# Performance work log

Measured on AMD Instinct MI355X. Metric: run time of the kernel, lower is better.

## Reference

```python
import jax, jax.numpy as jnp
import numpy as np

D_MODEL, N_HEADS, D_K, D_V, D_FF, SEQ = 2048, 16, 128, 128, 8192, 2048
EPS = 1e-5


def _layernorm(x, g, b):
    mu = jnp.mean(x, axis=-1, keepdims=True)
    var = jnp.var(x, axis=-1, keepdims=True)
    return (x - mu) * jax.lax.rsqrt(var + EPS) * g + b


def setup_inputs() -> dict:
    key = jax.random.key(0)
    ks = jax.random.split(key, 10)
    return {
        "x": jax.random.normal(ks[0], (SEQ, D_MODEL), jnp.float32),
        # per-head projections stacked over heads (matches num_heads separate DotProductAttention params)
        "wq": jax.random.normal(ks[1], (N_HEADS, D_MODEL, D_K), jnp.float32),
        "wk": jax.random.normal(ks[2], (N_HEADS, D_MODEL, D_K), jnp.float32),
        "wv": jax.random.normal(ks[3], (N_HEADS, D_MODEL, D_V), jnp.float32),
        "w_proj": jax.random.normal(ks[4], (N_HEADS * D_V, D_MODEL), jnp.float32),
        "g1": jnp.ones((D_MODEL,), jnp.float32),
        "b1": jnp.zeros((D_MODEL,), jnp.float32),
        "fc1_w": jax.random.normal(ks[5], (D_MODEL, D_FF), jnp.float32) * 0.02,
        "fc1_b": jnp.zeros((D_FF,), jnp.float32),
        "fc2_w": jax.random.normal(ks[6], (D_FF, D_MODEL), jnp.float32) * 0.02,
        "fc2_b": jnp.zeros((D_MODEL,), jnp.float32),
        "g2": jnp.ones((D_MODEL,), jnp.float32),
        "b2": jnp.zeros((D_MODEL,), jnp.float32),
    }


def reference(x, wq, wk, wv, w_proj, g1, b1, fc1_w, fc1_b, fc2_w, fc2_b, g2, b2):
    # multi-head attention (heads batched via einsum; same math as the per-head loop)
    q = jnp.einsum("sd,hdk->hsk", x, wq)
    k = jnp.einsum("sd,hdk->hsk", x, wk)
    v = jnp.einsum("sd,hdv->hsv", x, wv)
    scores = jnp.einsum("hsk,htk->hst", q, k) * (1.0 / np.sqrt(D_K))
    attn = jax.nn.softmax(scores, axis=-1)
    heads = jnp.einsum("hst,htv->hsv", attn, v)  # [H,S,Dv]
    concat = jnp.transpose(heads, (1, 0, 2)).reshape(SEQ, N_HEADS * D_V)
    attn_out = concat @ w_proj
    # residual + LayerNorm (dropout=0 -> identity)
    h = _layernorm(x + attn_out, g1, b1)
    # FFN with ReLU
    ff = jax.nn.relu(h @ fc1_w + fc1_b) @ fc2_w + fc2_b
    return _layernorm(h + ff, g2, b2)
```

## Files before the change

kernel.cpp:

```cpp
#include <hip/hip_runtime.h>


typedef __bf16 bf16;
typedef __attribute__((ext_vector_type(8))) __bf16 bf16x8;
typedef __attribute__((ext_vector_type(4))) __bf16 bf16x4;
typedef __attribute__((ext_vector_type(4))) float f32x4;
typedef __attribute__((ext_vector_type(4))) unsigned int u32x4;

#define MFMA(a, b, c) __builtin_amdgcn_mfma_f32_16x16x32_bf16((a), (b), (c), 0, 0, 0)
#define NEG_INF (-3.402823466e38f)

__device__ __forceinline__ void cp16(void* lds, const void* g) {
  __builtin_amdgcn_global_load_lds(
      (const __attribute__((address_space(1))) unsigned int*)g,
      (__attribute__((address_space(3))) unsigned int*)lds, 16, 0, 0);
}

#define SBAR() __builtin_amdgcn_sched_barrier(0)
#define GBAR()                              \
  do {                                      \
    asm volatile("" ::: "memory");          \
    __builtin_amdgcn_s_barrier();           \
    asm volatile("" ::: "memory");          \
  } while (0)
#define LGKM0()                                         \
  do {                                                  \
    asm volatile("s_waitcnt lgkmcnt(0)" ::: "memory");  \
    __builtin_amdgcn_sched_barrier(0);                  \
  } while (0)
#define VMC6()                                          \
  do {                                                  \
    asm volatile("s_waitcnt vmcnt(6)" ::: "memory");    \
    __builtin_amdgcn_sched_barrier(0);                  \
  } while (0)


__global__ void k_split_x(const float* __restrict__ x, bf16* __restrict__ xh,
                          bf16* __restrict__ xl) {
  int i = blockIdx.x * 256 + threadIdx.x;
  f32x4 v = ((const f32x4*)x)[i];
  bf16x4 h, l;
#pragma unroll
  for (int j = 0; j < 4; ++j) {
    bf16 hi = (bf16)v[j];
    h[j] = hi;
    l[j] = (bf16)(v[j] - (float)hi);
  }
  ((bf16x4*)xh)[i] = h;
  ((bf16x4*)xl)[i] = l;
}

template <bool SPLIT>
__global__ void k_tcvt(const float* __restrict__ in, bf16* __restrict__ oh,
                       bf16* __restrict__ ol, int R, int C) {
  __shared__ float t[64][65];
  long zoff = (long)blockIdx.z * R * C;
  int c0 = blockIdx.x * 64, r0 = blockIdx.y * 64;
  int cc = threadIdx.x & 63, rr = threadIdx.x >> 6;
#pragma unroll
  for (int i = 0; i < 16; ++i) {
    int r = i * 4 + rr;
    t[r][cc] = in[zoff + (long)(r0 + r) * C + c0 + cc];
  }
  __syncthreads();
#pragma unroll
  for (int i = 0; i < 16; ++i) {
    int orow = i * 4 + rr;
    float v = t[cc][orow];
    long oidx = zoff + (long)(c0 + orow) * R + r0 + cc;
    bf16 hi = (bf16)v;
    oh[oidx] = hi;
    if (SPLIT) ol[oidx] = (bf16)(v - (float)hi);
  }
}

__global__ void k_combine4(const float* __restrict__ p, long pstr,
                           bf16* __restrict__ o) {
  int i = blockIdx.x * 256 + threadIdx.x;
  f32x4 v = ((const f32x4*)p)[i];
#pragma unroll
  for (int zz = 1; zz < 4; ++zz) v += ((const f32x4*)(p + zz * pstr))[i];
  bf16x4 ob;
#pragma unroll
  for (int j = 0; j < 4; ++j) ob[j] = (bf16)v[j];
  ((bf16x4*)o)[i] = ob;
}

template <int EPI>
__global__ __launch_bounds__(512, 1) void k_gemm8(
    const bf16* __restrict__ A, const bf16* __restrict__ B,
    float* __restrict__ Cf, bf16* __restrict__ Cb,
    const float* __restrict__ bias, int M, int N, int K, int nsplit) {
  __shared__ char lds[131072];
  const int tid = threadIdx.x, w = tid >> 6, l = tid & 63;
  const int l16 = l & 15, lg = l >> 4;
  const int wr = w >> 2, wc = w & 3;
  const long bm0 = (long)blockIdx.y * 256, bn0 = (long)blockIdx.x * 256;
  const int z = blockIdx.z;
  const int ksz = K / nsplit, kbeg = z * ksz;
  const int nt = ksz >> 6;
  const long lK = K;

  const int srow = w * 8 + (l >> 3);
  const int sslot = (l & 7) ^ (l >> 3);

  auto STAGE = [&](int bufp, int isB, int h, int tt) {
    int tc = tt < nt ? tt : nt - 1;
    char* dst = lds + bufp * 65536 + isB * 32768 + h * 16384 + w * 1024;
    const bf16* G = isB ? B : A;
    long r0 = (isB ? bn0 : bm0) + h * 128 + srow;
    const bf16* src = G + r0 * lK + kbeg + tc * 64 + sslot * 8;
    cp16(dst, src);
    cp16(dst + 8192, src + 64 * lK);
  };
  auto LDA = [&](int bufp, int mf, int ks) -> bf16x8 {
    int inrow = (mf & 3) * 32 + wr * 16 + l16;
    int byo = bufp * 65536 + (mf >> 2) * 16384 + inrow * 128 +
              ((((ks << 2) + lg) ^ (inrow & 7)) << 4);
    return *(const bf16x8*)(lds + byo);
  };
  auto LDB = [&](int bufp, int nf, int ks) -> bf16x8 {
    int inrow = (nf & 1) * 64 + wc * 16 + l16;
    int byo = bufp * 65536 + 32768 + (nf >> 1) * 16384 + inrow * 128 +
              ((((ks << 2) + lg) ^ (inrow & 7)) << 4);
    return *(const bf16x8*)(lds + byo);
  };

  f32x4 acc[8][4];
#pragma unroll
  for (int mf = 0; mf < 8; ++mf)
#pragma unroll
    for (int nf = 0; nf < 4; ++nf)
#pragma unroll
      for (int j = 0; j < 4; ++j) acc[mf][nf][j] = 0.f;

  STAGE(0, 0, 0, 0);
  STAGE(0, 1, 0, 0);
  STAGE(0, 0, 1, 0);
  STAGE(0, 1, 1, 0);
  STAGE(1, 1, 0, 1);
  STAGE(1, 0, 1, 1);
  STAGE(1, 1, 1, 1);
  SBAR();
  VMC6();
  GBAR();

  bf16x8 a[4][2], b[2][2];
  for (int t = 0; t < nt; ++t) {
    const int cb = t & 1, nb = cb ^ 1;
#pragma unroll
    for (int mf = 0; mf < 4; ++mf)
#pragma unroll
      for (int ks = 0; ks < 2; ++ks) a[mf][ks] = LDA(cb, mf, ks);
#pragma unroll
    for (int nf = 0; nf < 2; ++nf)
#pragma unroll
      for (int ks = 0; ks < 2; ++ks) b[nf][ks] = LDB(cb, nf, ks);
    STAGE(nb, 0, 0, t + 1);
    SBAR();
    GBAR();
    LGKM0();
    __builtin_amdgcn_s_setprio(1);
#pragma unroll
    for (int mf = 0; mf < 4; ++mf)
#pragma unroll
      for (int nf = 0; nf < 2; ++nf)
#pragma unroll
        for (int ks = 0; ks < 2; ++ks)
          acc[mf][nf] = MFMA(a[mf][ks], b[nf][ks], acc[mf][nf]);
    __builtin_amdgcn_s_setprio(0);
    GBAR();
#pragma unroll
    for (int mf = 0; mf < 4; ++mf)
#pragma unroll
      for (int ks = 0; ks < 2; ++ks) a[mf][ks] = LDA(cb, mf + 4, ks);
    STAGE(cb, 1, 0, t + 2);
    SBAR();
    GBAR();
    LGKM0();
    __builtin_amdgcn_s_setprio(1);
#pragma unroll
    for (int mf = 0; mf < 4; ++mf)
#pragma unroll
      for (int nf = 0; nf < 2; ++nf)
#pragma unroll
        for (int ks = 0; ks < 2; ++ks)
          acc[mf + 4][nf] = MFMA(a[mf][ks], b[nf][ks], acc[mf + 4][nf]);
    __builtin_amdgcn_s_setprio(0);
    GBAR();
#pragma unroll
    for (int nf = 0; nf < 2; ++nf)
#pragma unroll
      for (int ks = 0; ks < 2; ++ks) b[nf][ks] = LDB(cb, nf + 2, ks);
    GBAR();
    LGKM0();
    __builtin_amdgcn_s_setprio(1);
#pragma unroll
    for (int mf = 0; mf < 4; ++mf)
#pragma unroll
      for (int nf = 0; nf < 2; ++nf)
#pragma unroll
        for (int ks = 0; ks < 2; ++ks)
          acc[mf + 4][nf + 2] = MFMA(a[mf][ks], b[nf][ks], acc[mf + 4][nf + 2]);
    __builtin_amdgcn_s_setprio(0);
    GBAR();
#pragma unroll
    for (int mf = 0; mf < 4; ++mf)
#pragma unroll
      for (int ks = 0; ks < 2; ++ks) a[mf][ks] = LDA(cb, mf, ks);
    STAGE(cb, 0, 1, t + 2);
    STAGE(cb, 1, 1, t + 2);
    SBAR();
    VMC6();
    GBAR();
    LGKM0();
    __builtin_amdgcn_s_setprio(1);
#pragma unroll
    for (int mf = 0; mf < 4; ++mf)
#pragma unroll
      for (int nf = 0; nf < 2; ++nf)
#pragma unroll
        for (int ks = 0; ks < 2; ++ks)
          acc[mf][nf + 2] = MFMA(a[mf][ks], b[nf][ks], acc[mf][nf + 2]);
    __builtin_amdgcn_s_setprio(0);
    GBAR();
  }
  asm volatile("s_waitcnt vmcnt(0) lgkmcnt(0)" ::: "memory");

#pragma unroll
  for (int mf = 0; mf < 8; ++mf)
#pragma unroll
    for (int nf = 0; nf < 4; ++nf) {
      long col = bn0 + nf * 64 + wc * 16 + l16;
      float bv = (EPI == 2) ? bias[col] : 0.f;
#pragma unroll
      for (int jj = 0; jj < 4; ++jj) {
        long row = bm0 + mf * 32 + wr * 16 + lg * 4 + jj;
        float v = acc[mf][nf][jj];
        if (EPI == 0) {
          Cf[(long)z * M * N + row * N + col] = v;
        } else {
          v = fmaxf(v + bv, 0.f);
          Cb[row * N + col] = (bf16)v;
        }
      }
    }
}

__global__ __launch_bounds__(512, 1) void k_split8(
    const bf16* __restrict__ Ah_g, const bf16* __restrict__ Al_g,
    const bf16* __restrict__ Bh_g, const bf16* __restrict__ Bl_g,
    bf16* __restrict__ Ch, bf16* __restrict__ Cl,
    int M, int N, int K, float scale, int scale_ncols) {
  __shared__ char lds[98304];
  const int tid = threadIdx.x, w = tid >> 6, l = tid & 63;
  const int l16 = l & 15, lg = l >> 4;
  const int wr = w >> 2, wc = w & 3;
  const long bm0 = (long)blockIdx.y * 128, bn0 = (long)blockIdx.x * 256;
  const int nt = K >> 5;
  const long lK = K;

  const int srcrow = tid >> 2;
  const int ss = (tid & 3) ^ ((tid >> 3) & 3);

  auto STG_A = [&](int bufp, int isLo, int tt) {
    int tc = tt < nt ? tt : nt - 1;
    char* dst = lds + bufp * 49152 + isLo * 8192 + tid * 16;
    const bf16* G = isLo ? Al_g : Ah_g;
    cp16(dst, &G[(bm0 + srcrow) * lK + tc * 32 + ss * 8]);
  };
  auto STG_B = [&](int bufp, int isLo, int half, int tt) {
    int tc = tt < nt ? tt : nt - 1;
    char* dst = lds + bufp * 49152 + 16384 + isLo * 16384 + half * 8192 + tid * 16;
    const bf16* G = isLo ? Bl_g : Bh_g;
    cp16(dst, &G[(bn0 + half * 128 + srcrow) * lK + tc * 32 + ss * 8]);
  };
  auto LDA8 = [&](int bufp, int mf, int isLo) -> bf16x8 {
    int row = mf * 32 + wr * 16 + l16;
    int byo = bufp * 49152 + isLo * 8192 + row * 64 +
              ((lg ^ ((row >> 1) & 3)) << 4);
    return *(const bf16x8*)(lds + byo);
  };
  auto LDB8 = [&](int bufp, int nf, int isLo) -> bf16x8 {
    int row = nf * 64 + wc * 16 + l16;
    int byo = bufp * 49152 + 16384 + isLo * 16384 + row * 64 +
              ((lg ^ ((row >> 1) & 3)) << 4);
    return *(const bf16x8*)(lds + byo);
  };

  f32x4 acc[4][4];
#pragma unroll
  for (int mf = 0; mf < 4; ++mf)
#pragma unroll
    for (int nf = 0; nf < 4; ++nf)
#pragma unroll
      for (int j = 0; j < 4; ++j) acc[mf][nf][j] = 0.f;

  STG_B(0, 0, 0, 0); STG_B(0, 1, 0, 0);
  STG_A(0, 0, 0);    STG_A(0, 1, 0);
  STG_B(0, 0, 1, 0); STG_B(0, 1, 1, 0);
  STG_B(1, 0, 0, 1); STG_B(1, 1, 0, 1);
  STG_A(1, 0, 1);    STG_A(1, 1, 1);
  STG_B(1, 0, 1, 1); STG_B(1, 1, 1, 1);
  SBAR();
  VMC6();
  GBAR();

  bf16x8 ah[4], al[4], bh[2], bl[2];
  for (int t = 0; t < nt; ++t) {
    const int cb = t & 1;
#pragma unroll
    for (int mf = 0; mf < 2; ++mf) {
      ah[mf] = LDA8(cb, mf, 0);
      al[mf] = LDA8(cb, mf, 1);
    }
#pragma unroll
    for (int nf = 0; nf < 2; ++nf) {
      bh[nf] = LDB8(cb, nf, 0);
      bl[nf] = LDB8(cb, nf, 1);
    }
    SBAR();
    GBAR();
    LGKM0();
    __builtin_amdgcn_s_setprio(1);
#pragma unroll
    for (int mf = 0; mf < 2; ++mf)
#pragma unroll
      for (int nf = 0; nf < 2; ++nf) {
        acc[mf][nf] = MFMA(ah[mf], bh[nf], acc[mf][nf]);
        acc[mf][nf] = MFMA(ah[mf], bl[nf], acc[mf][nf]);
        acc[mf][nf] = MFMA(al[mf], bh[nf], acc[mf][nf]);
      }
    __builtin_amdgcn_s_setprio(0);
    GBAR();
#pragma unroll
    for (int mf = 2; mf < 4; ++mf) {
      ah[mf] = LDA8(cb, mf, 0);
      al[mf] = LDA8(cb, mf, 1);
    }
    STG_B(cb, 0, 0, t + 2);
    STG_B(cb, 1, 0, t + 2);
    SBAR();
    GBAR();
    LGKM0();
    __builtin_amdgcn_s_setprio(1);
#pragma unroll
    for (int mf = 2; mf < 4; ++mf)
#pragma unroll
      for (int nf = 0; nf < 2; ++nf) {
        acc[mf][nf] = MFMA(ah[mf], bh[nf], acc[mf][nf]);
        acc[mf][nf] = MFMA(ah[mf], bl[nf], acc[mf][nf]);
        acc[mf][nf] = MFMA(al[mf], bh[nf], acc[mf][nf]);
      }
    __builtin_amdgcn_s_setprio(0);
    GBAR();
#pragma unroll
    for (int nf = 0; nf < 2; ++nf) {
      bh[nf] = LDB8(cb, nf + 2, 0);
      bl[nf] = LDB8(cb, nf + 2, 1);
    }
    STG_A(cb, 0, t + 2);
    STG_A(cb, 1, t + 2);
    SBAR();
    GBAR();
    LGKM0();
    __builtin_amdgcn_s_setprio(1);
#pragma unroll
    for (int mf = 2; mf < 4; ++mf)
#pragma unroll
      for (int nf = 0; nf < 2; ++nf) {
        acc[mf][nf + 2] = MFMA(ah[mf], bh[nf], acc[mf][nf + 2]);
        acc[mf][nf + 2] = MFMA(ah[mf], bl[nf], acc[mf][nf + 2]);
        acc[mf][nf + 2] = MFMA(al[mf], bh[nf], acc[mf][nf + 2]);
      }
    __builtin_amdgcn_s_setprio(0);
    GBAR();
    STG_B(cb, 0, 1, t + 2);
    STG_B(cb, 1, 1, t + 2);
    SBAR();
    VMC6();
    GBAR();
    __builtin_amdgcn_s_setprio(1);
#pragma unroll
    for (int mf = 0; mf < 2; ++mf)
#pragma unroll
      for (int nf = 0; nf < 2; ++nf) {
        acc[mf][nf + 2] = MFMA(ah[mf], bh[nf], acc[mf][nf + 2]);
        acc[mf][nf + 2] = MFMA(ah[mf], bl[nf], acc[mf][nf + 2]);
        acc[mf][nf + 2] = MFMA(al[mf], bh[nf], acc[mf][nf + 2]);
      }
    __builtin_amdgcn_s_setprio(0);
    GBAR();
  }
  asm volatile("s_waitcnt vmcnt(0) lgkmcnt(0)" ::: "memory");

#pragma unroll
  for (int mf = 0; mf < 4; ++mf)
#pragma unroll
    for (int nf = 0; nf < 4; ++nf) {
      long col = bn0 + nf * 64 + wc * 16 + l16;
      float sc = (col < scale_ncols) ? scale : 1.0f;
#pragma unroll
      for (int j = 0; j < 4; ++j) {
        long row = bm0 + mf * 32 + wr * 16 + lg * 4 + j;
        float v = acc[mf][nf][j] * sc;
        bf16 hi = (bf16)v;
        Ch[row * N + col] = hi;
        Cl[row * N + col] = (bf16)(v - (float)hi);
      }
    }
}

__global__ __launch_bounds__(256, 2) void k_flash(
    const bf16* __restrict__ Qh, const bf16* __restrict__ Ql,
    const bf16* __restrict__ Kh, const bf16* __restrict__ Kl,
    const bf16* __restrict__ Vt, bf16* __restrict__ Oc) {
  __shared__ bf16 sm[28672];
  bf16* sKh = sm;
  bf16* sKl = sm + 8192;
  bf16* sVt = sm + 16384;
  bf16* sP = sm + 24576;
  const int tid = threadIdx.x, w = tid >> 6, l = tid & 63;
  const int l16 = l & 15, lg = l >> 4;
  const int head = blockIdx.y;
  const long q0 = (long)blockIdx.x * 64;

  bf16x8 qh_r[4], ql_r[4];
#pragma unroll
  for (int kk = 0; kk < 4; ++kk) {
    long off = (q0 + w * 16 + l16) * 4096 + head * 128 + kk * 32 + lg * 8;
    qh_r[kk] = *(const bf16x8*)&Qh[off];
    ql_r[kk] = *(const bf16x8*)&Ql[off];
  }

  f32x4 acc_o[8];
#pragma unroll
  for (int n = 0; n < 8; ++n)
#pragma unroll
    for (int j = 0; j < 4; ++j) acc_o[n][j] = 0.f;
  float mrow[4], lrow[4];
#pragma unroll
  for (int j = 0; j < 4; ++j) {
    mrow[j] = NEG_INF;
    lrow[j] = 0.f;
  }

  auto LOADT = [&](u32x4 (&kh)[4], u32x4 (&kl)[4], u32x4 (&vt)[4], int t0) {
#pragma unroll
    for (int i = 0; i < 4; ++i) {
      int c = (w * 4 + i) * 64 + l;
      int rk = c >> 4, sk = (c & 15) ^ (rk & 7);
      long ko = (long)(t0 + rk) * 4096 + head * 128 + sk * 8;
      kh[i] = *(const u32x4*)&Kh[ko];
      kl[i] = *(const u32x4*)&Kl[ko];
      int rv = c >> 3, sv = (c & 7) ^ (rv & 7);
      long vo = (long)(head * 128 + rv) * 2048 + t0 + sv * 8;
      vt[i] = *(const u32x4*)&Vt[vo];
    }
  };
  auto WRITET = [&](u32x4 (&kh)[4], u32x4 (&kl)[4], u32x4 (&vt)[4]) {
#pragma unroll
    for (int i = 0; i < 4; ++i) {
      int db = (w * 4 + i) * 512 + l * 8;
      *(u32x4*)&sKh[db] = kh[i];
      *(u32x4*)&sKl[db] = kl[i];
      *(u32x4*)&sVt[db] = vt[i];
    }
  };
  auto COMPUTE = [&]() {
    f32x4 s[4];
#pragma unroll
    for (int n = 0; n < 4; ++n)
#pragma unroll
      for (int j = 0; j < 4; ++j) s[n][j] = 0.f;
#pragma unroll
    for (int kk = 0; kk < 4; ++kk) {
      bf16x8 bh[4], bl[4];
#pragma unroll
      for (int n = 0; n < 4; ++n) {
        int r = n * 16 + l16;
        int byo = r * 256 + (((kk * 4 + lg) ^ (r & 7)) << 4);
        bh[n] = *(const bf16x8*)((const char*)sKh + byo);
        bl[n] = *(const bf16x8*)((const char*)sKl + byo);
      }
#pragma unroll
      for (int n = 0; n < 4; ++n) {
        s[n] = MFMA(qh_r[kk], bh[n], s[n]);
        s[n] = MFMA(qh_r[kk], bl[n], s[n]);
        s[n] = MFMA(ql_r[kk], bh[n], s[n]);
      }
    }
#pragma unroll
    for (int j = 0; j < 4; ++j) {
      float mx = fmaxf(fmaxf(s[0][j], s[1][j]), fmaxf(s[2][j], s[3][j]));
      mx = fmaxf(mx, __shfl_xor(mx, 1));
      mx = fmaxf(mx, __shfl_xor(mx, 2));
      mx = fmaxf(mx, __shfl_xor(mx, 4));
      mx = fmaxf(mx, __shfl_xor(mx, 8));
      float mo = mrow[j];
      float mn = fmaxf(mo, mx);
      mrow[j] = mn;
      float f = __expf(mo - mn);
      int prow = w * 16 + lg * 4 + j;
      float ssum = 0.f;
#pragma unroll
      for (int n = 0; n < 4; ++n) {
        float p = __expf(s[n][j] - mn);
        ssum += p;
        int byo = prow * 128 + (((n * 16 + l16) * 2) ^ ((prow & 7) << 4));
        *(bf16*)((char*)sP + byo) = (bf16)p;
      }
      ssum += __shfl_xor(ssum, 1);
      ssum += __shfl_xor(ssum, 2);
      ssum += __shfl_xor(ssum, 4);
      ssum += __shfl_xor(ssum, 8);
      lrow[j] = lrow[j] * f + ssum;
#pragma unroll
      for (int n = 0; n < 8; ++n) acc_o[n][j] *= f;
    }
#pragma unroll
    for (int kk = 0; kk < 2; ++kk) {
      bf16x8 pa, bv[8];
      {
        int r = w * 16 + l16;
        int byo = r * 128 + (((kk * 4 + lg) ^ (r & 7)) << 4);
        pa = *(const bf16x8*)((const char*)sP + byo);
      }
#pragma unroll
      for (int n = 0; n < 8; ++n) {
        int r = n * 16 + l16;
        int byo = r * 128 + (((kk * 4 + lg) ^ (r & 7)) << 4);
        bv[n] = *(const bf16x8*)((const char*)sVt + byo);
      }
#pragma unroll
      for (int n = 0; n < 8; ++n) acc_o[n] = MFMA(pa, bv[n], acc_o[n]);
    }
  };

  u32x4 akh[4], akl[4], avt[4], bkh[4], bkl[4], bvt[4];
  LOADT(akh, akl, avt, 0);
  for (int tt = 0; tt < 2048; tt += 128) {
    __syncthreads();
    WRITET(akh, akl, avt);
    __syncthreads();
    LOADT(bkh, bkl, bvt, tt + 64);
    COMPUTE();
    __syncthreads();
    WRITET(bkh, bkl, bvt);
    __syncthreads();
    LOADT(akh, akl, avt, (tt + 128 < 2048) ? tt + 128 : 0);
    COMPUTE();
  }

#pragma unroll
  for (int j = 0; j < 4; ++j) {
    float rinv = 1.f / lrow[j];
    long row = q0 + w * 16 + lg * 4 + j;
#pragma unroll
    for (int n = 0; n < 8; ++n)
      Oc[row * 2048 + head * 128 + n * 16 + l16] = (bf16)(acc_o[n][j] * rinv);
  }
}

__global__ __launch_bounds__(256) void k_add_ln(
    const float* __restrict__ a, const float* __restrict__ p, long pstr,
    int np, const float* __restrict__ bias, const float* __restrict__ g,
    const float* __restrict__ be, float* __restrict__ o32,
    bf16* __restrict__ obf) {
  __shared__ float red[8];
  int row = blockIdx.x, tid = threadIdx.x;
  const float* pa = a + (long)row * 2048;
  f32x4 v[2];
  float sum = 0.f, sq = 0.f;
#pragma unroll
  for (int i = 0; i < 2; ++i) {
    int idx = i * 1024 + tid * 4;
    v[i] = *(const f32x4*)(pa + idx);
    for (int zz = 0; zz < np; ++zz)
      v[i] += *(const f32x4*)(p + zz * pstr + (long)row * 2048 + idx);
    if (bias != nullptr) v[i] += *(const f32x4*)(bias + idx);
#pragma unroll
    for (int j = 0; j < 4; ++j) {
      sum += v[i][j];
      sq += v[i][j] * v[i][j];
    }
  }
#pragma unroll
  for (int o = 1; o < 64; o <<= 1) {
    sum += __shfl_xor(sum, o);
    sq += __shfl_xor(sq, o);
  }
  int w = tid >> 6;
  if ((tid & 63) == 0) {
    red[w * 2] = sum;
    red[w * 2 + 1] = sq;
  }
  __syncthreads();
  sum = red[0] + red[2] + red[4] + red[6];
  sq = red[1] + red[3] + red[5] + red[7];
  float mu = sum * (1.f / 2048.f);
  float var = sq * (1.f / 2048.f) - mu * mu;
  float rs = rsqrtf(var + 1e-5f);
#pragma unroll
  for (int i = 0; i < 2; ++i) {
    int idx = i * 1024 + tid * 4;
    f32x4 vg = *(const f32x4*)(g + idx);
    f32x4 vb = *(const f32x4*)(be + idx);
    f32x4 o;
#pragma unroll
    for (int j = 0; j < 4; ++j) o[j] = (v[i][j] - mu) * rs * vg[j] + vb[j];
    *(f32x4*)(o32 + (long)row * 2048 + idx) = o;
    if (obf != nullptr) {
      bf16x4 ob;
#pragma unroll
      for (int j = 0; j < 4; ++j) ob[j] = (bf16)o[j];
      *(bf16x4*)(obf + (long)row * 2048 + idx) = ob;
    }
  }
}

extern "C" void kernel_launch(void* const* d_in, const int* in_sizes, int n_in,
                              void* d_out, int out_size, void* d_ws, size_t ws_size,
                              hipStream_t stream) {
  const float* x    = (const float*)d_in[0];
  const float* wq   = (const float*)d_in[1];
  const float* wk   = (const float*)d_in[2];
  const float* wv   = (const float*)d_in[3];
  const float* wp   = (const float*)d_in[4];
  const float* g1   = (const float*)d_in[5];
  const float* b1   = (const float*)d_in[6];
  const float* fc1w = (const float*)d_in[7];
  const float* fc1b = (const float*)d_in[8];
  const float* fc2w = (const float*)d_in[9];
  const float* fc2b = (const float*)d_in[10];
  const float* g2   = (const float*)d_in[11];
  const float* b2   = (const float*)d_in[12];
  float* out = (float*)d_out;

  char* ws = (char*)d_ws;
  const size_t MB = 1024 * 1024;
  if (ws_size < 216 * MB) return;
  const long W4M = 4L * 1024 * 1024;

  bf16* xh    = (bf16*)(ws + 0 * MB);
  bf16* xl    = (bf16*)(ws + 8 * MB);
  bf16* qk_bh = (bf16*)(ws + 16 * MB);
  bf16* qk_bl = (bf16*)(ws + 32 * MB);
  bf16* wvt   = (bf16*)(ws + 48 * MB);
  bf16* wpt   = (bf16*)(ws + 56 * MB);
  bf16* fc1t  = (bf16*)(ws + 64 * MB);
  bf16* fc2t  = (bf16*)(ws + 96 * MB);
  float* vtp  = (float*)(ws + 128 * MB);
  bf16* vtb   = (bf16*)(ws + 192 * MB);
  bf16* qkh   = (bf16*)(ws + 128 * MB);
  bf16* qkl   = (bf16*)(ws + 144 * MB);
  bf16* cc    = (bf16*)(ws + 200 * MB);
  float* aop  = (float*)(ws + 128 * MB);
  float* h32  = (float*)(ws + 192 * MB);
  bf16*  hbf  = (bf16*)(ws + 208 * MB);
  bf16*  ff1  = (bf16*)(ws + 128 * MB);
  float* ffp  = (float*)(ws + 0 * MB);
  const long PSTR = 4194304L;

  k_split_x<<<4096, 256, 0, stream>>>(x, xh, xl);
  k_tcvt<true ><<<dim3(2, 32, 16), 256, 0, stream>>>(wq, qk_bh, qk_bl, 2048, 128);
  k_tcvt<true ><<<dim3(2, 32, 16), 256, 0, stream>>>(wk, qk_bh + W4M, qk_bl + W4M,
                                                     2048, 128);
  k_tcvt<false><<<dim3(2, 32, 16), 256, 0, stream>>>(wv, wvt, nullptr, 2048, 128);
  k_tcvt<false><<<dim3(32, 32, 1), 256, 0, stream>>>(wp, wpt, nullptr, 2048, 2048);
  k_tcvt<false><<<dim3(128, 32, 1), 256, 0, stream>>>(fc1w, fc1t, nullptr, 2048, 8192);
  k_tcvt<false><<<dim3(32, 128, 1), 256, 0, stream>>>(fc2w, fc2t, nullptr, 8192, 2048);

  k_gemm8<0><<<dim3(8, 8, 4), 512, 0, stream>>>(
      wvt, xh, vtp, nullptr, nullptr, 2048, 2048, 2048, 4);
  k_combine4<<<4096, 256, 0, stream>>>(vtp, PSTR, vtb);
  k_split8<<<dim3(16, 16), 512, 0, stream>>>(
      xh, xl, qk_bh, qk_bl, qkh, qkl, 2048, 4096, 2048,
      0.08838834764831845f, 2048);
  k_flash<<<dim3(32, 16), 256, 0, stream>>>(qkh, qkl, qkh + 2048, qkl + 2048,
                                            vtb, cc);
  k_gemm8<0><<<dim3(8, 8, 4), 512, 0, stream>>>(
      cc, wpt, aop, nullptr, nullptr, 2048, 2048, 2048, 4);
  k_add_ln<<<2048, 256, 0, stream>>>(x, aop, PSTR, 4, nullptr, g1, b1, h32, hbf);
  k_gemm8<2><<<dim3(32, 8, 1), 512, 0, stream>>>(
      hbf, fc1t, nullptr, ff1, fc1b, 2048, 8192, 2048, 1);
  k_gemm8<0><<<dim3(8, 8, 4), 512, 0, stream>>>(
      ff1, fc2t, ffp, nullptr, nullptr, 2048, 2048, 8192, 4);
  k_add_ln<<<2048, 256, 0, stream>>>(h32, ffp, PSTR, 4, fc2b, g2, b2, out, nullptr);
}
```

Measured before the change: 543.3 us.

## Load flash-attention K/V tiles directly to LDS and alias P buffer for occupancy

The flash attention kernel drops its register-staged double-buffered K/V prefetch and instead issues global_load_lds copies straight into shared memory each 64-key tile. The softmax P buffer now reuses the Kl region after an extra barrier, which shrinks LDS per block. Launch bounds rise to three blocks per CU, and s_setprio wraps the MFMA sections. The goal is higher occupancy and lower register pressure so other waves hide latency, at the cost of losing explicit load/compute overlap within a block and adding a barrier per tile.

New measurement: 515.7 us. 1.05x faster.

```diff
diff --git a/kernel.cpp b/kernel.cpp
--- a/kernel.cpp
+++ b/kernel.cpp
@@ -5,7 +5,6 @@
 typedef __attribute__((ext_vector_type(8))) __bf16 bf16x8;
 typedef __attribute__((ext_vector_type(4))) __bf16 bf16x4;
 typedef __attribute__((ext_vector_type(4))) float f32x4;
-typedef __attribute__((ext_vector_type(4))) unsigned int u32x4;
 
 #define MFMA(a, b, c) __builtin_amdgcn_mfma_f32_16x16x32_bf16((a), (b), (c), 0, 0, 0)
 #define NEG_INF (-3.402823466e38f)
@@ -411,15 +410,15 @@
     }
 }
 
-__global__ __launch_bounds__(256, 2) void k_flash(
+__global__ __launch_bounds__(256, 3) void k_flash(
     const bf16* __restrict__ Qh, const bf16* __restrict__ Ql,
     const bf16* __restrict__ Kh, const bf16* __restrict__ Kl,
     const bf16* __restrict__ Vt, bf16* __restrict__ Oc) {
-  __shared__ bf16 sm[28672];
+  __shared__ bf16 sm[24576];
   bf16* sKh = sm;
   bf16* sKl = sm + 8192;
   bf16* sVt = sm + 16384;
-  bf16* sP = sm + 24576;
+  bf16* sP = sKl;
   const int tid = threadIdx.x, w = tid >> 6, l = tid & 63;
   const int l16 = l & 15, lg = l >> 4;
   const int head = blockIdx.y;
@@ -445,34 +444,28 @@
     lrow[j] = 0.f;
   }
 
-  auto LOADT = [&](u32x4 (&kh)[4], u32x4 (&kl)[4], u32x4 (&vt)[4], int t0) {
+  for (int t0 = 0; t0 < 2048; t0 += 64) {
+    __syncthreads();
 #pragma unroll
     for (int i = 0; i < 4; ++i) {
       int c = (w * 4 + i) * 64 + l;
       int rk = c >> 4, sk = (c & 15) ^ (rk & 7);
       long ko = (long)(t0 + rk) * 4096 + head * 128 + sk * 8;
-      kh[i] = *(const u32x4*)&Kh[ko];
-      kl[i] = *(const u32x4*)&Kl[ko];
+      int db = (w * 4 + i) * 512;
+      cp16(&sKh[db], &Kh[ko]);
+      cp16(&sKl[db], &Kl[ko]);
       int rv = c >> 3, sv = (c & 7) ^ (rv & 7);
       long vo = (long)(head * 128 + rv) * 2048 + t0 + sv * 8;
-      vt[i] = *(const u32x4*)&Vt[vo];
-    }
-  };
-  auto WRITET = [&](u32x4 (&kh)[4], u32x4 (&kl)[4], u32x4 (&vt)[4]) {
-#pragma unroll
-    for (int i = 0; i < 4; ++i) {
-      int db = (w * 4 + i) * 512 + l * 8;
-      *(u32x4*)&sKh[db] = kh[i];
-      *(u32x4*)&sKl[db] = kl[i];
-      *(u32x4*)&sVt[db] = vt[i];
-    }
-  };
-  auto COMPUTE = [&]() {
+      cp16(&sVt[db], &Vt[vo]);
+    }
+    __syncthreads();
+
     f32x4 s[4];
 #pragma unroll
     for (int n = 0; n < 4; ++n)
 #pragma unroll
       for (int j = 0; j < 4; ++j) s[n][j] = 0.f;
+    __builtin_amdgcn_s_setprio(1);
 #pragma unroll
     for (int kk = 0; kk < 4; ++kk) {
       bf16x8 bh[4], bl[4];
@@ -490,6 +483,9 @@
         s[n] = MFMA(ql_r[kk], bh[n], s[n]);
       }
     }
+    __builtin_amdgcn_s_setprio(0);
+    __syncthreads();
+
 #pragma unroll
     for (int j = 0; j < 4; ++j) {
       float mx = fmaxf(fmaxf(s[0][j], s[1][j]), fmaxf(s[2][j], s[3][j]));
@@ -518,6 +514,8 @@
 #pragma unroll
       for (int n = 0; n < 8; ++n) acc_o[n][j] *= f;
     }
+
+    __builtin_amdgcn_s_setprio(1);
 #pragma unroll
     for (int kk = 0; kk < 2; ++kk) {
       bf16x8 pa, bv[8];
@@ -535,21 +533,7 @@
 #pragma unroll
       for (int n = 0; n < 8; ++n) acc_o[n] = MFMA(pa, bv[n], acc_o[n]);
     }
-  };
-
-  u32x4 akh[4], akl[4], avt[4], bkh[4], bkl[4], bvt[4];
-  LOADT(akh, akl, avt, 0);
-  for (int tt = 0; tt < 2048; tt += 128) {
-    __syncthreads();
-    WRITET(akh, akl, avt);
-    __syncthreads();
-    LOADT(bkh, bkl, bvt, tt + 64);
-    COMPUTE();
-    __syncthreads();
-    WRITET(bkh, bkl, bvt);
-    __syncthreads();
-    LOADT(akh, akl, avt, (tt + 128 < 2048) ? tt + 128 : 0);
-    COMPUTE();
+    __builtin_amdgcn_s_setprio(0);
   }
 
 #pragma unroll
```
